# Performance work log

Hardware: AMD Instinct MI355X
Metric: run time of the kernel (lower is better)

Reference implementation:

```python
import jax, jax.numpy as jnp
import numpy as np
from jax import lax

EPS = 1e-7  # keras K.epsilon()
DN = ('NHWC', 'HWIO', 'NHWC')


def _box_avg(z, k):
    """Depthwise k x k box filter with SAME padding, scaled by 1/(k*k*C).
    Matches tf.nn.depthwise_conv2d with a ones/(k*k*C) kernel, implemented
    separably (two 1D convs) for efficiency."""
    C = z.shape[-1]
    scale = 1.0 / (k * k * C)  # note: keras code divides by full kernel size incl. C
    kh = jnp.ones((k, 1, 1, C), z.dtype)
    kw = jnp.ones((1, k, 1, C), z.dtype)
    z = lax.conv_general_dilated(z, kh, (1, 1), 'SAME',
                                 dimension_numbers=DN, feature_group_count=C)
    z = lax.conv_general_dilated(z, kw, (1, 1), 'SAME',
                                 dimension_numbers=DN, feature_group_count=C)
    return z * scale


def setup_inputs() -> dict:
    key = jax.random.key(0)
    x = jax.random.normal(key, (8, 1024, 1024, 2), dtype=jnp.float32)
    return {"x": x, "filter_size": 61}


def reference(x, filter_size):
    k = int(filter_size)
    # norm_method == 'std':
    out = x - _box_avg(x, k)                       # local mean-subtract
    c1 = _box_avg(out, k)
    c2 = _box_avg(out * out, k)
    std = jnp.sqrt(c2 - c1 * c1) + EPS             # local window std
    return out / std
```

## Files before the change

kernel.cpp:

```cpp
#include <hip/hip_runtime.h>
#include <math.h>

#define NB 8
#define HH 1024
#define WW 1024
#define RAD 30
#define KS 61
#define ROWSZ 2048
#define IMGSZ (HH * ROWSZ)
#define STR2 1024
#define NCOL2 (NB * STR2)
#define VSEGH 32
#define VNSEG (HH / VSEGH)
#define EPSV 1e-7f
#define SCALEV (1.0f / (float)(KS * KS * 2))
#define PDW (WW + WW / 8)
#define PD(i) ((i) + ((i) >> 3))

__device__ __forceinline__ unsigned bf16_rn(float f) {
    unsigned u = __float_as_uint(f);
    return (u + 0x7FFFu + ((u >> 16) & 1u)) >> 16;
}
__device__ __forceinline__ unsigned pk2(float a, float b) {
    return bf16_rn(a) | (bf16_rn(b) << 16);
}
__device__ __forceinline__ float2 up2(unsigned u) {
    return make_float2(__uint_as_float(u << 16),
                       __uint_as_float(u & 0xFFFF0000u));
}

__device__ __forceinline__ float2 f2add(float2 a, float2 b) {
    return make_float2(a.x + b.x, a.y + b.y);
}
__device__ __forceinline__ float2 f2sub(float2 a, float2 b) {
    return make_float2(a.x - b.x, a.y - b.y);
}

__global__ __launch_bounds__(256, 4) void vbox_kernel(const float* __restrict__ in,
                                                      unsigned* __restrict__ out) {
    int tid = blockIdx.x * 256 + threadIdx.x;
    int col = tid & (NCOL2 - 1);
    int seg = tid >> 13;
    int n = col >> 10;
    int w2 = col & (STR2 - 1);
    const float2* ip = (const float2*)(in + (size_t)n * IMGSZ) + w2;
    unsigned* op = out + (size_t)n * (IMGSZ / 2) + w2;
    int h0 = seg * VSEGH;
    float2 S = make_float2(0.f, 0.f);
    int lo = h0 - RAD; if (lo < 0) lo = 0;
    int h = lo;
    for (; h + 4 <= h0 + RAD; h += 4) {
        float2 v0 = ip[(h + 0) * STR2];
        float2 v1 = ip[(h + 1) * STR2];
        float2 v2 = ip[(h + 2) * STR2];
        float2 v3 = ip[(h + 3) * STR2];
        S = f2add(S, f2add(f2add(v0, v1), f2add(v2, v3)));
    }
    for (; h < h0 + RAD; ++h) S = f2add(S, ip[h * STR2]);

    if (seg != 0 && seg != VNSEG - 1) {
        const float2* lp = ip + (h0 + RAD) * STR2;
        const float2* tp = ip + (h0 - RAD) * STR2;
        unsigned* opp = op + (size_t)h0 * STR2;
        for (int r = 0; r < VSEGH; r += 8) {
            float2 L[8], T[8];
            #pragma unroll
            for (int i = 0; i < 8; ++i) L[i] = lp[(r + i) * STR2];
            #pragma unroll
            for (int i = 0; i < 8; ++i) T[i] = tp[(r + i) * STR2];
            #pragma unroll
            for (int i = 0; i < 8; ++i) {
                S = f2add(S, L[i]);
                opp[(r + i) * STR2] = pk2(S.x, S.y);
                S = f2sub(S, T[i]);
            }
        }
    } else {
        const float2 Z = make_float2(0.f, 0.f);
        for (int ho = h0; ho < h0 + VSEGH; ho += 4) {
            float2 a[4], b[4];
            #pragma unroll
            for (int i = 0; i < 4; ++i) {
                int ha = ho + i + RAD;
                a[i] = (ha < HH) ? ip[ha * STR2] : Z;
            }
            #pragma unroll
            for (int i = 0; i < 4; ++i) {
                int hb = ho + i - RAD;
                b[i] = (hb >= 0) ? ip[hb * STR2] : Z;
            }
            #pragma unroll
            for (int i = 0; i < 4; ++i) {
                S = f2add(S, a[i]);
                op[(size_t)(ho + i) * STR2] = pk2(S.x, S.y);
                S = f2sub(S, b[i]);
            }
        }
    }
}

__global__ __launch_bounds__(256, 4) void vbox2_kernel(const float* __restrict__ in,
                                                       unsigned* __restrict__ o1,
                                                       unsigned* __restrict__ o2) {
    int tid = blockIdx.x * 256 + threadIdx.x;
    int col = tid & (NCOL2 - 1);
    int seg = tid >> 13;
    int n = col >> 10;
    int w2 = col & (STR2 - 1);
    const float2* ip = (const float2*)(in + (size_t)n * IMGSZ) + w2;
    unsigned* p1 = o1 + (size_t)n * (IMGSZ / 2) + w2;
    unsigned* p2 = o2 + (size_t)n * (IMGSZ / 2) + w2;
    int h0 = seg * VSEGH;
    float2 S = make_float2(0.f, 0.f);
    float2 Q = make_float2(0.f, 0.f);
    int lo = h0 - RAD; if (lo < 0) lo = 0;
    int h = lo;
    for (; h + 4 <= h0 + RAD; h += 4) {
        float2 v0 = ip[(h + 0) * STR2];
        float2 v1 = ip[(h + 1) * STR2];
        float2 v2 = ip[(h + 2) * STR2];
        float2 v3 = ip[(h + 3) * STR2];
        S = f2add(S, f2add(f2add(v0, v1), f2add(v2, v3)));
        Q.x = fmaf(v0.x, v0.x, fmaf(v1.x, v1.x, fmaf(v2.x, v2.x, fmaf(v3.x, v3.x, Q.x))));
        Q.y = fmaf(v0.y, v0.y, fmaf(v1.y, v1.y, fmaf(v2.y, v2.y, fmaf(v3.y, v3.y, Q.y))));
    }
    for (; h < h0 + RAD; ++h) {
        float2 v = ip[h * STR2];
        S = f2add(S, v);
        Q.x = fmaf(v.x, v.x, Q.x); Q.y = fmaf(v.y, v.y, Q.y);
    }

    if (seg != 0 && seg != VNSEG - 1) {
        const float2* lp = ip + (h0 + RAD) * STR2;
        const float2* tp = ip + (h0 - RAD) * STR2;
        unsigned* q1 = p1 + (size_t)h0 * STR2;
        unsigned* q2 = p2 + (size_t)h0 * STR2;
        for (int r = 0; r < VSEGH; r += 8) {
            float2 L[8], T[8];
            #pragma unroll
            for (int i = 0; i < 8; ++i) L[i] = lp[(r + i) * STR2];
            #pragma unroll
            for (int i = 0; i < 8; ++i) T[i] = tp[(r + i) * STR2];
            #pragma unroll
            for (int i = 0; i < 8; ++i) {
                S = f2add(S, L[i]);
                Q.x = fmaf(L[i].x, L[i].x, Q.x);
                Q.y = fmaf(L[i].y, L[i].y, Q.y);
                q1[(r + i) * STR2] = pk2(S.x, S.y);
                q2[(r + i) * STR2] = pk2(Q.x, Q.y);
                S = f2sub(S, T[i]);
                Q.x = fmaf(-T[i].x, T[i].x, Q.x);
                Q.y = fmaf(-T[i].y, T[i].y, Q.y);
            }
        }
    } else {
        const float2 Z = make_float2(0.f, 0.f);
        for (int ho = h0; ho < h0 + VSEGH; ho += 4) {
            float2 a[4], b[4];
            #pragma unroll
            for (int i = 0; i < 4; ++i) {
                int ha = ho + i + RAD;
                a[i] = (ha < HH) ? ip[ha * STR2] : Z;
            }
            #pragma unroll
            for (int i = 0; i < 4; ++i) {
                int hb = ho + i - RAD;
                b[i] = (hb >= 0) ? ip[hb * STR2] : Z;
            }
            #pragma unroll
            for (int i = 0; i < 4; ++i) {
                S = f2add(S, a[i]);
                Q.x = fmaf(a[i].x, a[i].x, Q.x);
                Q.y = fmaf(a[i].y, a[i].y, Q.y);
                p1[(size_t)(ho + i) * STR2] = pk2(S.x, S.y);
                p2[(size_t)(ho + i) * STR2] = pk2(Q.x, Q.y);
                S = f2sub(S, b[i]);
                Q.x = fmaf(-b[i].x, b[i].x, Q.x);
                Q.y = fmaf(-b[i].y, b[i].y, Q.y);
            }
        }
    }
}

__device__ inline float wave_incl_scan(float v) {
    int lane = threadIdx.x & 63;
    #pragma unroll
    for (int d = 1; d < 64; d <<= 1) {
        float o = __shfl_up(v, d, 64);
        if (lane >= d) v += o;
    }
    return v;
}

__global__ __launch_bounds__(256) void hbox_sub_kernel(const unsigned* __restrict__ vsum,
                                                       const float* __restrict__ x,
                                                       float* __restrict__ out) {
    __shared__ float ch[2][PDW];
    __shared__ float wtot[4];
    int t = threadIdx.x;
    size_t g = (size_t)blockIdx.x * ROWSZ;
    const uint4* vrow = (const uint4*)(vsum + (size_t)blockIdx.x * STR2);
    uint4 u = vrow[t];
    {
        float2 p0 = up2(u.x), p1 = up2(u.y), p2 = up2(u.z), p3 = up2(u.w);
        int w = 4 * t;
        ch[0][PD(w + 0)] = p0.x; ch[1][PD(w + 0)] = p0.y;
        ch[0][PD(w + 1)] = p1.x; ch[1][PD(w + 1)] = p1.y;
        ch[0][PD(w + 2)] = p2.x; ch[1][PD(w + 2)] = p2.y;
        ch[0][PD(w + 3)] = p3.x; ch[1][PD(w + 3)] = p3.y;
    }
    __syncthreads();
    {
        int c = t >> 7, j = t & 127, base = j * 8;
        float v[8]; float run = 0.f;
        #pragma unroll
        for (int i = 0; i < 8; ++i) { run += ch[c][PD(base + i)]; v[i] = run; }
        float incl = wave_incl_scan(run);
        int wid = t >> 6;
        if ((t & 63) == 63) wtot[wid] = incl;
        __syncthreads();
        float off = incl - run;
        if (wid & 1) off += wtot[wid - 1];
        #pragma unroll
        for (int i = 0; i < 8; ++i) ch[c][PD(base + i)] = off + v[i];
    }
    __syncthreads();
    const float4* xrow = (const float4*)(x + g);
    float4* orow = (float4*)(out + g);
    #pragma unroll
    for (int i = 0; i < 2; ++i) {
        int jj = t + 256 * i;
        int w0 = 2 * jj, w1 = 2 * jj + 1;
        int hi0 = w0 + RAD; if (hi0 > WW - 1) hi0 = WW - 1;
        int hi1 = w1 + RAD; if (hi1 > WW - 1) hi1 = WW - 1;
        int lo0 = w0 - RAD - 1, lo1 = w1 - RAD - 1;
        float s00 = ch[0][PD(hi0)], s10 = ch[1][PD(hi0)];
        if (lo0 >= 0) { s00 -= ch[0][PD(lo0)]; s10 -= ch[1][PD(lo0)]; }
        float s01 = ch[0][PD(hi1)], s11 = ch[1][PD(hi1)];
        if (lo1 >= 0) { s01 -= ch[0][PD(lo1)]; s11 -= ch[1][PD(lo1)]; }
        float4 xv = xrow[jj];
        float4 o;
        o.x = xv.x - SCALEV * s00; o.y = xv.y - SCALEV * s10;
        o.z = xv.z - SCALEV * s01; o.w = xv.w - SCALEV * s11;
        orow[jj] = o;
    }
}

__global__ __launch_bounds__(256) void hbox_final_kernel(const unsigned* __restrict__ z1,
                                                         const unsigned* __restrict__ z2,
                                                         float* __restrict__ out) {
    __shared__ float ch[4][PDW];
    int t = threadIdx.x;
    size_t g = (size_t)blockIdx.x * ROWSZ;
    const uint4* arow = (const uint4*)(z1 + (size_t)blockIdx.x * STR2);
    const uint4* brow = (const uint4*)(z2 + (size_t)blockIdx.x * STR2);
    uint4 ua = arow[t], ub = brow[t];
    {
        float2 p0 = up2(ua.x), p1 = up2(ua.y), p2 = up2(ua.z), p3 = up2(ua.w);
        float2 q0 = up2(ub.x), q1 = up2(ub.y), q2 = up2(ub.z), q3 = up2(ub.w);
        int w = 4 * t;
        ch[0][PD(w + 0)] = p0.x; ch[1][PD(w + 0)] = p0.y;
        ch[0][PD(w + 1)] = p1.x; ch[1][PD(w + 1)] = p1.y;
        ch[0][PD(w + 2)] = p2.x; ch[1][PD(w + 2)] = p2.y;
        ch[0][PD(w + 3)] = p3.x; ch[1][PD(w + 3)] = p3.y;
        ch[2][PD(w + 0)] = q0.x; ch[3][PD(w + 0)] = q0.y;
        ch[2][PD(w + 1)] = q1.x; ch[3][PD(w + 1)] = q1.y;
        ch[2][PD(w + 2)] = q2.x; ch[3][PD(w + 2)] = q2.y;
        ch[2][PD(w + 3)] = q3.x; ch[3][PD(w + 3)] = q3.y;
    }
    __syncthreads();
    {
        int a = t >> 6, j = t & 63, base = j * 16;
        float v[16]; float run = 0.f;
        #pragma unroll
        for (int i = 0; i < 16; ++i) { run += ch[a][PD(base + i)]; v[i] = run; }
        float incl = wave_incl_scan(run);
        float off = incl - run;
        #pragma unroll
        for (int i = 0; i < 16; ++i) ch[a][PD(base + i)] = off + v[i];
    }
    __syncthreads();
    float4* orow = (float4*)(out + g);
    #pragma unroll
    for (int i = 0; i < 2; ++i) {
        int jj = t + 256 * i;
        int w0 = 2 * jj, w1 = 2 * jj + 1;
        int hi0 = w0 + RAD; if (hi0 > WW - 1) hi0 = WW - 1;
        int hi1 = w1 + RAD; if (hi1 > WW - 1) hi1 = WW - 1;
        int lo0 = w0 - RAD - 1, lo1 = w1 - RAD - 1;
        float s1a = ch[0][PD(hi0)], s1b = ch[1][PD(hi0)];
        float s2a = ch[2][PD(hi0)], s2b = ch[3][PD(hi0)];
        if (lo0 >= 0) {
            s1a -= ch[0][PD(lo0)]; s1b -= ch[1][PD(lo0)];
            s2a -= ch[2][PD(lo0)]; s2b -= ch[3][PD(lo0)];
        }
        float s1c = ch[0][PD(hi1)], s1d = ch[1][PD(hi1)];
        float s2c = ch[2][PD(hi1)], s2d = ch[3][PD(hi1)];
        if (lo1 >= 0) {
            s1c -= ch[0][PD(lo1)]; s1d -= ch[1][PD(lo1)];
            s2c -= ch[2][PD(lo1)]; s2d -= ch[3][PD(lo1)];
        }
        float4 ov = orow[jj];
        float c1, c2, var;
        float4 r;
        c1 = SCALEV * s1a; c2 = SCALEV * s2a; var = c2 - c1 * c1;
        r.x = ov.x / (sqrtf(fmaxf(var, 0.f)) + EPSV);
        c1 = SCALEV * s1b; c2 = SCALEV * s2b; var = c2 - c1 * c1;
        r.y = ov.y / (sqrtf(fmaxf(var, 0.f)) + EPSV);
        c1 = SCALEV * s1c; c2 = SCALEV * s2c; var = c2 - c1 * c1;
        r.z = ov.z / (sqrtf(fmaxf(var, 0.f)) + EPSV);
        c1 = SCALEV * s1d; c2 = SCALEV * s2d; var = c2 - c1 * c1;
        r.w = ov.w / (sqrtf(fmaxf(var, 0.f)) + EPSV);
        orow[jj] = r;
    }
}

extern "C" void kernel_launch(void* const* d_in, const int* in_sizes, int n_in,
                              void* d_out, int out_size, void* d_ws, size_t ws_size,
                              hipStream_t stream) {
    const float* x = (const float*)d_in[0];
    float* out = (float*)d_out;
    unsigned* V1 = (unsigned*)d_ws;
    unsigned* Z1 = V1 + (size_t)NB * IMGSZ / 2;
    unsigned* Z2 = Z1 + (size_t)NB * IMGSZ / 2;

    int vgrid = (NCOL2 * VNSEG) / 256;
    vbox_kernel<<<vgrid, 256, 0, stream>>>(x, V1);
    hbox_sub_kernel<<<NB * HH, 256, 0, stream>>>(V1, x, out);
    vbox2_kernel<<<vgrid, 256, 0, stream>>>(out, Z1, Z2);
    hbox_final_kernel<<<NB * HH, 256, 0, stream>>>(Z1, Z2, out);
}
```

Measured before the change: 219.0 us.

## Lengthen vertical box segments, batch warm-up loads, pin load scheduling

After: 213.9 us. -2.3%, faster.

```diff
diff --git a/kernel.cpp b/kernel.cpp
--- a/kernel.cpp
+++ b/kernel.cpp
@@ -10,7 +10,7 @@
 #define IMGSZ (HH * ROWSZ)
 #define STR2 1024
 #define NCOL2 (NB * STR2)
-#define VSEGH 32
+#define VSEGH 64
 #define VNSEG (HH / VSEGH)
 #define EPSV 1e-7f
 #define SCALEV (1.0f / (float)(KS * KS * 2))
@@ -36,7 +36,7 @@
     return make_float2(a.x - b.x, a.y - b.y);
 }
 
-__global__ __launch_bounds__(256, 4) void vbox_kernel(const float* __restrict__ in,
+__global__ __launch_bounds__(256, 2) void vbox_kernel(const float* __restrict__ in,
                                                       unsigned* __restrict__ out) {
     int tid = blockIdx.x * 256 + threadIdx.x;
     int col = tid & (NCOL2 - 1);
@@ -49,12 +49,13 @@
     float2 S = make_float2(0.f, 0.f);
     int lo = h0 - RAD; if (lo < 0) lo = 0;
     int h = lo;
-    for (; h + 4 <= h0 + RAD; h += 4) {
-        float2 v0 = ip[(h + 0) * STR2];
-        float2 v1 = ip[(h + 1) * STR2];
-        float2 v2 = ip[(h + 2) * STR2];
-        float2 v3 = ip[(h + 3) * STR2];
-        S = f2add(S, f2add(f2add(v0, v1), f2add(v2, v3)));
+    for (; h + 8 <= h0 + RAD; h += 8) {
+        float2 W[8];
+        #pragma unroll
+        for (int i = 0; i < 8; ++i) W[i] = ip[(h + i) * STR2];
+        __builtin_amdgcn_sched_barrier(0);
+        #pragma unroll
+        for (int i = 0; i < 8; ++i) S = f2add(S, W[i]);
     }
     for (; h < h0 + RAD; ++h) S = f2add(S, ip[h * STR2]);
 
@@ -68,6 +69,7 @@
             for (int i = 0; i < 8; ++i) L[i] = lp[(r + i) * STR2];
             #pragma unroll
             for (int i = 0; i < 8; ++i) T[i] = tp[(r + i) * STR2];
+            __builtin_amdgcn_sched_barrier(0);
             #pragma unroll
             for (int i = 0; i < 8; ++i) {
                 S = f2add(S, L[i]);
@@ -99,7 +101,7 @@
     }
 }
 
-__global__ __launch_bounds__(256, 4) void vbox2_kernel(const float* __restrict__ in,
+__global__ __launch_bounds__(256, 2) void vbox2_kernel(const float* __restrict__ in,
                                                        unsigned* __restrict__ o1,
                                                        unsigned* __restrict__ o2) {
     int tid = blockIdx.x * 256 + threadIdx.x;
@@ -115,14 +117,17 @@
     float2 Q = make_float2(0.f, 0.f);
     int lo = h0 - RAD; if (lo < 0) lo = 0;
     int h = lo;
-    for (; h + 4 <= h0 + RAD; h += 4) {
-        float2 v0 = ip[(h + 0) * STR2];
-        float2 v1 = ip[(h + 1) * STR2];
-        float2 v2 = ip[(h + 2) * STR2];
-        float2 v3 = ip[(h + 3) * STR2];
-        S = f2add(S, f2add(f2add(v0, v1), f2add(v2, v3)));
-        Q.x = fmaf(v0.x, v0.x, fmaf(v1.x, v1.x, fmaf(v2.x, v2.x, fmaf(v3.x, v3.x, Q.x))));
-        Q.y = fmaf(v0.y, v0.y, fmaf(v1.y, v1.y, fmaf(v2.y, v2.y, fmaf(v3.y, v3.y, Q.y))));
+    for (; h + 8 <= h0 + RAD; h += 8) {
+        float2 W[8];
+        #pragma unroll
+        for (int i = 0; i < 8; ++i) W[i] = ip[(h + i) * STR2];
+        __builtin_amdgcn_sched_barrier(0);
+        #pragma unroll
+        for (int i = 0; i < 8; ++i) {
+            S = f2add(S, W[i]);
+            Q.x = fmaf(W[i].x, W[i].x, Q.x);
+            Q.y = fmaf(W[i].y, W[i].y, Q.y);
+        }
     }
     for (; h < h0 + RAD; ++h) {
         float2 v = ip[h * STR2];
@@ -141,6 +146,7 @@
             for (int i = 0; i < 8; ++i) L[i] = lp[(r + i) * STR2];
             #pragma unroll
             for (int i = 0; i < 8; ++i) T[i] = tp[(r + i) * STR2];
+            __builtin_amdgcn_sched_barrier(0);
             #pragma unroll
             for (int i = 0; i < 8; ++i) {
                 S = f2add(S, L[i]);
```
